# Kernel tuning notes

Hardware: AMD Instinct MI355X
Metric: run time of the kernel (lower is better)

## Reference

```python
import jax, jax.numpy as jnp
import numpy as np

S = 7
B = 2
C = 80
N = 8192
LAMBD_COORD = 5.0
LAMBD_NOOBJ = 0.5


def setup_inputs() -> dict:
    key = jax.random.key(0)
    k1, k2, k3 = jax.random.split(key, 3)
    prediction = jax.random.uniform(k1, (N, S, S, B * 5 + C), dtype=jnp.float32)
    target = jax.random.uniform(k2, (N, S, S, 5 + C), dtype=jnp.float32)
    conf = (jax.random.uniform(k3, (N, S, S)) > 0.7).astype(jnp.float32)
    target = target.at[..., 4].set(conf)
    return {"prediction": prediction, "target": target}


def _rel2abs(box):
    # box: (N,S,S,>=4) with (xcr_rcell, ycr_rcell, wr, hr); returns corner coords (image-relative)
    x, y, w, h = box[..., 0], box[..., 1], box[..., 2], box[..., 3]
    jj = jnp.arange(S, dtype=box.dtype)[None, None, :]   # cell_j -> x axis
    ii = jnp.arange(S, dtype=box.dtype)[None, :, None]   # cell_i -> y axis
    xc = (x + jj) / S
    yc = (y + ii) / S
    return xc - w / 2, yc - h / 2, xc + w / 2, yc + h / 2


def _iou(a, b):
    ax1, ay1, ax2, ay2 = a
    bx1, by1, bx2, by2 = b
    iw = jnp.clip(jnp.minimum(ax2, bx2) - jnp.maximum(ax1, bx1), 0.0)
    ih = jnp.clip(jnp.minimum(ay2, by2) - jnp.maximum(ay1, by1), 0.0)
    inter = iw * ih
    area_a = (ax2 - ax1) * (ay2 - ay1)
    area_b = (bx2 - bx1) * (by2 - by1)
    return inter / (area_a + area_b - inter + 1e-6)


def reference(prediction, target):
    tgt_abs = _rel2abs(target[..., :5])
    iou0 = _iou(tgt_abs, _rel2abs(prediction[..., 0:5]))
    iou1 = _iou(tgt_abs, _rel2abs(prediction[..., 5:10]))
    # faithful to source: mask True (iou0 > iou1) selects offset idx = 5 (second box)
    sel_mask = (iou0 > iou1)[..., None]                              # (N,S,S,1)
    box_sel = jnp.where(sel_mask, prediction[..., 5:10], prediction[..., 0:5])
    xy_hat = box_sel[..., 0:2]
    wh_hat = box_sel[..., 2:4]

    xy = target[..., 0:2]
    wh = target[..., 2:4]
    # faithful to source: pred_c uses box_k after the loop, i.e. 4 + 5*(B-1)
    pred_c = prediction[..., 4 + 5 * (B - 1)]
    true_c = target[..., 4]

    obj = (true_c != 0)                  # contributions kept where object present
    objf = obj.astype(prediction.dtype)
    noobjf = 1.0 - objf

    # xy loss
    loss_xy_cell = objf * jnp.sum((xy - xy_hat) ** 2, axis=-1)

    # wh loss with sqrt-safe masking (masked entries contribute 0, matching masked_fill)
    obj_e = obj[..., None]
    wh_safe = jnp.where(obj_e, wh, 1.0)
    wh_hat_safe = jnp.where(obj_e, jnp.maximum(wh_hat, 0.0), 1.0)
    loss_wh_cell = objf * jnp.sum((jnp.sqrt(wh_safe) - jnp.sqrt(wh_hat_safe)) ** 2, axis=-1)

    # confidence losses
    conf_se = (true_c - pred_c) ** 2
    loss_conf_obj_cell = objf * conf_se
    loss_conf_noobj_cell = noobjf * conf_se

    # class loss
    pred_class = prediction[..., 5 * B:]
    true_class = target[..., 5:]
    loss_class_cell = objf * jnp.sum((true_class - pred_class) ** 2, axis=-1)

    bs = prediction.shape[0]
    loss_xy = jnp.sum(loss_xy_cell) / bs
    loss_wh = jnp.sum(loss_wh_cell) / bs
    loss_conf_obj = jnp.sum(loss_conf_obj_cell) / bs
    loss_conf_noobj = jnp.sum(loss_conf_noobj_cell) / bs
    loss_class = jnp.sum(loss_class_cell) / bs

    # faithful to source: weighted sum divided by BATCH_SIZE once more
    loss = (LAMBD_COORD * loss_xy + LAMBD_COORD * loss_wh + loss_conf_obj
            + LAMBD_NOOBJ * loss_conf_noobj + loss_class) / bs
    return loss, loss_xy, loss_wh, loss_conf_obj, loss_conf_noobj, loss_class
```

## Files before the change

### kernel.cpp

```cpp
#include <hip/hip_runtime.h>


#define NCELLS (8192 * 49)
#define NTILES (NCELLS / 64)
#define NBLOCKS (NTILES / 4)
constexpr float BSF = 8192.0f;

__device__ __forceinline__ void g2lds16(const float* g, float* s) {
    __builtin_amdgcn_global_load_lds(
        (const __attribute__((address_space(1))) void*)g,
        (__attribute__((address_space(3))) void*)s,
        16, 0, 0);
}

__device__ __forceinline__ void rel2abs(float x, float y, float w, float h,
                                        float fi, float fj,
                                        float& x1, float& y1, float& x2, float& y2) {
    float xc = (x + fj) / 7.0f;
    float yc = (y + fi) / 7.0f;
    float hw = w * 0.5f, hh = h * 0.5f;
    x1 = xc - hw; y1 = yc - hh; x2 = xc + hw; y2 = yc + hh;
}

__device__ __forceinline__ float iou_abs(float ax1, float ay1, float ax2, float ay2,
                                         float bx1, float by1, float bx2, float by2) {
    float iw = fminf(ax2, bx2) - fmaxf(ax1, bx1); iw = fmaxf(iw, 0.0f);
    float ih = fminf(ay2, by2) - fmaxf(ay1, by1); ih = fmaxf(ih, 0.0f);
    float inter  = iw * ih;
    float area_a = (ax2 - ax1) * (ay2 - ay1);
    float area_b = (bx2 - bx1) * (by2 - by1);
    return inter / (area_a + area_b - inter + 1e-6f);
}

__global__ __launch_bounds__(256) void yolo_main(const float* __restrict__ pred,
                                                 const float* __restrict__ tgt,
                                                 float* __restrict__ acc) {
    __shared__ __align__(16) float t_s[5440];
    __shared__ __align__(16) float p_s[5760];
    __shared__ float smr[4 * 5];

    const int tid  = threadIdx.x;
    const int lane = tid & 63;
    const int wid  = tid >> 6;

    float a_xy = 0.f, a_wh = 0.f, a_co = 0.f, a_cn = 0.f, a_cl = 0.f;

    const int tile0 = blockIdx.x * 4;

    for (int it = 0; it < 4; ++it) {
        const int tile = tile0 + it;
        const int base = tile << 6;

        const float* gtb = tgt  + (size_t)base * 85;
        const float* gpb = pred + (size_t)base * 90;

        #pragma unroll
        for (int i = 0; i < 5; ++i) {
            int idx = 4 * (tid + 256 * i);
            g2lds16(gtb + idx, t_s + idx);
        }
        if (tid < 80) {
            int idx = 4 * (tid + 1280);
            g2lds16(gtb + idx, t_s + idx);
        }
        #pragma unroll
        for (int i = 0; i < 5; ++i) {
            int idx = 4 * (tid + 256 * i);
            g2lds16(gpb + idx, p_s + idx);
        }
        if (tid < 160) {
            int idx = 4 * (tid + 1280);
            g2lds16(gpb + idx, p_s + idx);
        }

        __syncthreads();

        const float* tr = t_s + 85 * lane;
        const float* pr = p_s + 90 * lane;

        if (wid == 0) {
            float tx = tr[0], ty = tr[1], tw = tr[2], th = tr[3], tc = tr[4];
            float p0x = pr[0], p0y = pr[1], p0w = pr[2], p0h = pr[3];
            float p1x = pr[5], p1y = pr[6], p1w = pr[7], p1h = pr[8];
            float pc  = pr[9];

            float objf = (tc != 0.0f) ? 1.0f : 0.0f;

            int cell = base + lane;
            int sij  = cell % 49;
            float fi = (float)(sij / 7);
            float fj = (float)(sij % 7);

            float t1, t2, t3, t4, a1, a2, a3, a4, b1, b2, b3, b4;
            rel2abs(tx,  ty,  tw,  th,  fi, fj, t1, t2, t3, t4);
            rel2abs(p0x, p0y, p0w, p0h, fi, fj, a1, a2, a3, a4);
            rel2abs(p1x, p1y, p1w, p1h, fi, fj, b1, b2, b3, b4);

            float iou0 = iou_abs(t1, t2, t3, t4, a1, a2, a3, a4);
            float iou1 = iou_abs(t1, t2, t3, t4, b1, b2, b3, b4);

            bool sel = iou0 > iou1;
            float xh = sel ? p1x : p0x;
            float yh = sel ? p1y : p0y;
            float wh = sel ? p1w : p0w;
            float hh = sel ? p1h : p0h;

            float dx = tx - xh, dy = ty - yh;
            a_xy += objf * (dx * dx + dy * dy);

            float sw = sqrtf(tw) - sqrtf(fmaxf(wh, 0.0f));
            float sh = sqrtf(th) - sqrtf(fmaxf(hh, 0.0f));
            a_wh += objf * (sw * sw + sh * sh);

            float ce = tc - pc; ce *= ce;
            a_co += objf * ce;
            a_cn += (1.0f - objf) * ce;
        } else {
            float objf = (tr[4] != 0.0f) ? 1.0f : 0.0f;
            const int c0 = (wid == 1) ? 0  : (wid == 2) ? 27 : 54;
            const int c1 = (wid == 1) ? 27 : (wid == 2) ? 54 : 80;
            float s = 0.f;
            #pragma unroll 9
            for (int ch = c0; ch < c1; ++ch) {
                float d = tr[5 + ch] - pr[10 + ch];
                s += d * d;
            }
            a_cl += objf * s;
        }
        __syncthreads();
    }

    #pragma unroll
    for (int off = 32; off; off >>= 1) {
        a_xy += __shfl_down(a_xy, off, 64);
        a_wh += __shfl_down(a_wh, off, 64);
        a_co += __shfl_down(a_co, off, 64);
        a_cn += __shfl_down(a_cn, off, 64);
        a_cl += __shfl_down(a_cl, off, 64);
    }
    if (lane == 0) {
        smr[wid * 5 + 0] = a_xy; smr[wid * 5 + 1] = a_wh; smr[wid * 5 + 2] = a_co;
        smr[wid * 5 + 3] = a_cn; smr[wid * 5 + 4] = a_cl;
    }
    __syncthreads();
    if (tid == 0) {
        float s0 = 0.f, s1 = 0.f, s2 = 0.f, s3 = 0.f, s4 = 0.f;
        #pragma unroll
        for (int w = 0; w < 4; ++w) {
            s0 += smr[w * 5 + 0]; s1 += smr[w * 5 + 1]; s2 += smr[w * 5 + 2];
            s3 += smr[w * 5 + 3]; s4 += smr[w * 5 + 4];
        }
        atomicAdd(&acc[0], s0);
        atomicAdd(&acc[1], s1);
        atomicAdd(&acc[2], s2);
        atomicAdd(&acc[3], s3);
        atomicAdd(&acc[4], s4);
    }
}

__global__ void yolo_finalize(const float* __restrict__ acc, float* __restrict__ out) {
    if (threadIdx.x == 0 && blockIdx.x == 0) {
        float lxy = acc[0] / BSF;
        float lwh = acc[1] / BSF;
        float lco = acc[2] / BSF;
        float lcn = acc[3] / BSF;
        float lcl = acc[4] / BSF;
        out[0] = (5.0f * lxy + 5.0f * lwh + lco + 0.5f * lcn + lcl) / BSF;
        out[1] = lxy;
        out[2] = lwh;
        out[3] = lco;
        out[4] = lcn;
        out[5] = lcl;
    }
}

extern "C" void kernel_launch(void* const* d_in, const int* in_sizes, int n_in,
                              void* d_out, int out_size, void* d_ws, size_t ws_size,
                              hipStream_t stream) {
    const float* pred = (const float*)d_in[0];
    const float* tgt  = (const float*)d_in[1];
    float* out = (float*)d_out;
    float* acc = (float*)d_ws;

    hipMemsetAsync(acc, 0, 5 * sizeof(float), stream);

    yolo_main<<<NBLOCKS, 256, 0, stream>>>(pred, tgt, acc);
    yolo_finalize<<<1, 64, 0, stream>>>(acc, out);
}
```

Before: 335.2 us.

## Double-buffer LDS tiles, balance work across waves, spread atomics over replicas

Switches to 32-cell tiles staged into two LDS buffers, so the next tile's global-to-LDS loads are issued while the current one is computed, with manual vmcnt waits and raw barriers. The class loss is split evenly across all four waves, and the box/IoU work rotates between waves instead of always landing on wave 0. Accumulator atomics are spread over up to 8 padded replicas, which the finalize kernel sums. This targets load latency and wave imbalance, and relies on a hand-set vmcnt count and on the raw barriers keeping the buffers correctly ordered.

```diff
diff --git a/kernel.cpp b/kernel.cpp
--- a/kernel.cpp
+++ b/kernel.cpp
@@ -2,8 +2,17 @@
 
 
 #define NCELLS (8192 * 49)
-#define NTILES (NCELLS / 64)
-#define NBLOCKS (NTILES / 4)
+#define TILE_CELLS 32
+#define NTILES (NCELLS / TILE_CELLS)
+#define TPB 8
+#define NBLOCKS (NTILES / TPB)
+#define T_FLOATS (TILE_CELLS * 85)
+#define P_FLOATS (TILE_CELLS * 90)
+#define BUF_FLOATS (T_FLOATS + P_FLOATS)
+#define T_CHUNKS (T_FLOATS / 4)
+#define TOT_CHUNKS (BUF_FLOATS / 4)
+#define W_CHUNKS (TOT_CHUNKS / 4)
+
 constexpr float BSF = 8192.0f;
 
 __device__ __forceinline__ void g2lds16(const float* g, float* s) {
@@ -32,11 +41,33 @@
     return inter / (area_a + area_b - inter + 1e-6f);
 }
 
+__device__ __forceinline__ void stage_tile(const float* __restrict__ pred,
+                                           const float* __restrict__ tgt,
+                                           float* lbuf, int tile,
+                                           int wid, int lane) {
+    const float* tg = tgt  + (size_t)tile * T_FLOATS;
+    const float* pg = pred + (size_t)tile * P_FLOATS;
+    #pragma unroll
+    for (int i = 0; i < 5; ++i) {
+        const int q = W_CHUNKS * wid + 64 * i + lane;
+        const float* src = (q < T_CHUNKS) ? (tg + 4 * q) : (pg + 4 * (q - T_CHUNKS));
+        g2lds16(src, lbuf + 4 * q);
+    }
+    {
+        const int cw = 320 + lane;
+        if (cw < W_CHUNKS) {
+            const int q = W_CHUNKS * wid + cw;
+            const float* src = (q < T_CHUNKS) ? (tg + 4 * q) : (pg + 4 * (q - T_CHUNKS));
+            g2lds16(src, lbuf + 4 * q);
+        }
+    }
+}
+
 __global__ __launch_bounds__(256) void yolo_main(const float* __restrict__ pred,
                                                  const float* __restrict__ tgt,
-                                                 float* __restrict__ acc) {
-    __shared__ __align__(16) float t_s[5440];
-    __shared__ __align__(16) float p_s[5760];
+                                                 float* __restrict__ acc,
+                                                 int nrep, int sstride) {
+    __shared__ __align__(16) float lds[2][BUF_FLOATS];
     __shared__ float smr[4 * 5];
 
     const int tid  = threadIdx.x;
@@ -45,89 +76,80 @@
 
     float a_xy = 0.f, a_wh = 0.f, a_co = 0.f, a_cn = 0.f, a_cl = 0.f;
 
-    const int tile0 = blockIdx.x * 4;
-
-    for (int it = 0; it < 4; ++it) {
-        const int tile = tile0 + it;
-        const int base = tile << 6;
-
-        const float* gtb = tgt  + (size_t)base * 85;
-        const float* gpb = pred + (size_t)base * 90;
-
-        #pragma unroll
-        for (int i = 0; i < 5; ++i) {
-            int idx = 4 * (tid + 256 * i);
-            g2lds16(gtb + idx, t_s + idx);
-        }
-        if (tid < 80) {
-            int idx = 4 * (tid + 1280);
-            g2lds16(gtb + idx, t_s + idx);
-        }
-        #pragma unroll
-        for (int i = 0; i < 5; ++i) {
-            int idx = 4 * (tid + 256 * i);
-            g2lds16(gpb + idx, p_s + idx);
-        }
-        if (tid < 160) {
-            int idx = 4 * (tid + 1280);
-            g2lds16(gpb + idx, p_s + idx);
-        }
-
-        __syncthreads();
-
-        const float* tr = t_s + 85 * lane;
-        const float* pr = p_s + 90 * lane;
-
-        if (wid == 0) {
-            float tx = tr[0], ty = tr[1], tw = tr[2], th = tr[3], tc = tr[4];
-            float p0x = pr[0], p0y = pr[1], p0w = pr[2], p0h = pr[3];
-            float p1x = pr[5], p1y = pr[6], p1w = pr[7], p1h = pr[8];
-            float pc  = pr[9];
-
-            float objf = (tc != 0.0f) ? 1.0f : 0.0f;
-
-            int cell = base + lane;
-            int sij  = cell % 49;
-            float fi = (float)(sij / 7);
-            float fj = (float)(sij % 7);
-
-            float t1, t2, t3, t4, a1, a2, a3, a4, b1, b2, b3, b4;
-            rel2abs(tx,  ty,  tw,  th,  fi, fj, t1, t2, t3, t4);
-            rel2abs(p0x, p0y, p0w, p0h, fi, fj, a1, a2, a3, a4);
-            rel2abs(p1x, p1y, p1w, p1h, fi, fj, b1, b2, b3, b4);
-
-            float iou0 = iou_abs(t1, t2, t3, t4, a1, a2, a3, a4);
-            float iou1 = iou_abs(t1, t2, t3, t4, b1, b2, b3, b4);
-
-            bool sel = iou0 > iou1;
-            float xh = sel ? p1x : p0x;
-            float yh = sel ? p1y : p0y;
-            float wh = sel ? p1w : p0w;
-            float hh = sel ? p1h : p0h;
-
-            float dx = tx - xh, dy = ty - yh;
-            a_xy += objf * (dx * dx + dy * dy);
-
-            float sw = sqrtf(tw) - sqrtf(fmaxf(wh, 0.0f));
-            float sh = sqrtf(th) - sqrtf(fmaxf(hh, 0.0f));
-            a_wh += objf * (sw * sw + sh * sh);
-
-            float ce = tc - pc; ce *= ce;
-            a_co += objf * ce;
-            a_cn += (1.0f - objf) * ce;
+    const int tile0 = blockIdx.x * TPB;
+
+    stage_tile(pred, tgt, &lds[0][0], tile0, wid, lane);
+
+    for (int it = 0; it < TPB; ++it) {
+        if (it + 1 < TPB) {
+            stage_tile(pred, tgt, &lds[(it + 1) & 1][0], tile0 + it + 1, wid, lane);
+            asm volatile("s_waitcnt vmcnt(6)" ::: "memory");
         } else {
-            float objf = (tr[4] != 0.0f) ? 1.0f : 0.0f;
-            const int c0 = (wid == 1) ? 0  : (wid == 2) ? 27 : 54;
-            const int c1 = (wid == 1) ? 27 : (wid == 2) ? 54 : 80;
+            asm volatile("s_waitcnt vmcnt(0)" ::: "memory");
+        }
+        __builtin_amdgcn_s_barrier();
+        asm volatile("" ::: "memory");
+
+        {
+            const float* buf  = &lds[it & 1][0];
+            const int   cell  = lane & 31;
+            const int   half  = lane >> 5;
+            const float* tb   = buf + 85 * cell;
+            const float* pb   = buf + T_FLOATS + 90 * cell;
+
+            const float objf = (tb[4] != 0.0f) ? 1.0f : 0.0f;
+
+            const int c0 = 20 * wid + 10 * half;
             float s = 0.f;
-            #pragma unroll 9
-            for (int ch = c0; ch < c1; ++ch) {
-                float d = tr[5 + ch] - pr[10 + ch];
-                s += d * d;
+            #pragma unroll
+            for (int k = 0; k < 10; ++k) {
+                float d = tb[5 + c0 + k] - pb[10 + c0 + k];
+                s = fmaf(d, d, s);
             }
             a_cl += objf * s;
-        }
-        __syncthreads();
+
+            if (half == 0 && wid == (it & 3)) {
+                float tx = tb[0], ty = tb[1], tw = tb[2], th = tb[3], tc = tb[4];
+                float p0x = pb[0], p0y = pb[1], p0w = pb[2], p0h = pb[3];
+                float p1x = pb[5], p1y = pb[6], p1w = pb[7], p1h = pb[8];
+                float pc  = pb[9];
+
+                int gcell = (tile0 + it) * TILE_CELLS + cell;
+                int sij   = gcell % 49;
+                float fi  = (float)(sij / 7);
+                float fj  = (float)(sij % 7);
+
+                float t1, t2, t3, t4, a1, a2, a3, a4, b1, b2, b3, b4;
+                rel2abs(tx,  ty,  tw,  th,  fi, fj, t1, t2, t3, t4);
+                rel2abs(p0x, p0y, p0w, p0h, fi, fj, a1, a2, a3, a4);
+                rel2abs(p1x, p1y, p1w, p1h, fi, fj, b1, b2, b3, b4);
+
+                float iou0 = iou_abs(t1, t2, t3, t4, a1, a2, a3, a4);
+                float iou1 = iou_abs(t1, t2, t3, t4, b1, b2, b3, b4);
+
+                bool sel = iou0 > iou1;
+                float xh = sel ? p1x : p0x;
+                float yh = sel ? p1y : p0y;
+                float wh = sel ? p1w : p0w;
+                float hh = sel ? p1h : p0h;
+
+                float obx = (tc != 0.0f) ? 1.0f : 0.0f;
+
+                float dx = tx - xh, dy = ty - yh;
+                a_xy += obx * (dx * dx + dy * dy);
+
+                float sw = sqrtf(tw) - sqrtf(fmaxf(wh, 0.0f));
+                float sh = sqrtf(th) - sqrtf(fmaxf(hh, 0.0f));
+                a_wh += obx * (sw * sw + sh * sh);
+
+                float ce = tc - pc; ce *= ce;
+                a_co += obx * ce;
+                a_cn += (1.0f - obx) * ce;
+            }
+        }
+
+        asm volatile("" ::: "memory");
+        __builtin_amdgcn_s_barrier();
     }
 
     #pragma unroll
@@ -150,21 +172,28 @@
             s0 += smr[w * 5 + 0]; s1 += smr[w * 5 + 1]; s2 += smr[w * 5 + 2];
             s3 += smr[w * 5 + 3]; s4 += smr[w * 5 + 4];
         }
-        atomicAdd(&acc[0], s0);
-        atomicAdd(&acc[1], s1);
-        atomicAdd(&acc[2], s2);
-        atomicAdd(&acc[3], s3);
-        atomicAdd(&acc[4], s4);
-    }
-}
-
-__global__ void yolo_finalize(const float* __restrict__ acc, float* __restrict__ out) {
+        const int rep = (int)(blockIdx.x & (unsigned)(nrep - 1));
+        float* a0 = acc + (size_t)rep * 5 * sstride;
+        atomicAdd(&a0[0 * sstride], s0);
+        atomicAdd(&a0[1 * sstride], s1);
+        atomicAdd(&a0[2 * sstride], s2);
+        atomicAdd(&a0[3 * sstride], s3);
+        atomicAdd(&a0[4 * sstride], s4);
+    }
+}
+
+__global__ void yolo_finalize(const float* __restrict__ acc, float* __restrict__ out,
+                              int nrep, int sstride) {
     if (threadIdx.x == 0 && blockIdx.x == 0) {
-        float lxy = acc[0] / BSF;
-        float lwh = acc[1] / BSF;
-        float lco = acc[2] / BSF;
-        float lcn = acc[3] / BSF;
-        float lcl = acc[4] / BSF;
+        float s[5] = {0.f, 0.f, 0.f, 0.f, 0.f};
+        for (int r = 0; r < nrep; ++r)
+            for (int k = 0; k < 5; ++k)
+                s[k] += acc[((size_t)r * 5 + k) * sstride];
+        float lxy = s[0] / BSF;
+        float lwh = s[1] / BSF;
+        float lco = s[2] / BSF;
+        float lcn = s[3] / BSF;
+        float lcl = s[4] / BSF;
         out[0] = (5.0f * lxy + 5.0f * lwh + lco + 0.5f * lcn + lcl) / BSF;
         out[1] = lxy;
         out[2] = lwh;
@@ -182,8 +211,12 @@
     float* out = (float*)d_out;
     float* acc = (float*)d_ws;
 
-    hipMemsetAsync(acc, 0, 5 * sizeof(float), stream);
-
-    yolo_main<<<NBLOCKS, 256, 0, stream>>>(pred, tgt, acc);
-    yolo_finalize<<<1, 64, 0, stream>>>(acc, out);
-}
+    int nrep, sstride; size_t zbytes;
+    if (ws_size >= 8 * 5 * 32 * sizeof(float)) { nrep = 8; sstride = 32; zbytes = 8 * 5 * 32 * sizeof(float); }
+    else                                       { nrep = 1; sstride = 1;  zbytes = 5 * sizeof(float); }
+
+    hipMemsetAsync(acc, 0, zbytes, stream);
+
+    yolo_main<<<NBLOCKS, 256, 0, stream>>>(pred, tgt, acc, nrep, sstride);
+    yolo_finalize<<<1, 64, 0, stream>>>(acc, out, nrep, sstride);
+}
```

Result: faster. 309.7 us (-7.6%).
